# Kernel optimization log

Hardware: AMD Instinct MI355X
Metric: run time of the kernel (lower is better)

## Reference

```python
import jax, jax.numpy as jnp
import numpy as np

HIDDEN = 1024
NUM_HEADS = 16
GROUP_SIZE = 2
GROUP_NUM = NUM_HEADS // GROUP_SIZE
HEAD_DIM = HIDDEN // NUM_HEADS


def setup_inputs() -> dict:
    key = jax.random.key(0)
    ks = jax.random.split(key, 9)
    B, S = 1, 4096
    s = 0.02
    return {
        "hidden_state": jax.random.normal(ks[0], (B, S, HIDDEN), jnp.float32),
        "Wq": jax.random.normal(ks[1], (HIDDEN, HIDDEN), jnp.float32) * s,
        "bq": jnp.zeros((HIDDEN,), jnp.float32),
        "Wk": jax.random.normal(ks[2], (HIDDEN, GROUP_NUM * HEAD_DIM), jnp.float32) * s,
        "bk": jnp.zeros((GROUP_NUM * HEAD_DIM,), jnp.float32),
        "Wv": jax.random.normal(ks[3], (HIDDEN, GROUP_NUM * HEAD_DIM), jnp.float32) * s,
        "bv": jnp.zeros((GROUP_NUM * HEAD_DIM,), jnp.float32),
        "Wo": jax.random.normal(ks[4], (HIDDEN, HIDDEN), jnp.float32) * s,
        "bo": jnp.zeros((HIDDEN,), jnp.float32),
    }


def reference(hidden_state, Wq, bq, Wk, bk, Wv, bv, Wo, bo):
    B, S, _ = hidden_state.shape
    # projections
    q = hidden_state @ Wq + bq                      # [B,S,H*hd]
    k = hidden_state @ Wk + bk                      # [B,S,G*hd]
    v = hidden_state @ Wv + bv                      # [B,S,G*hd]
    q = q.reshape(B, S, NUM_HEADS, HEAD_DIM).transpose(0, 2, 1, 3)   # [B,H,S,hd]
    k = k.reshape(B, S, GROUP_NUM, HEAD_DIM).transpose(0, 2, 1, 3)   # [B,G,S,hd]
    v = v.reshape(B, S, GROUP_NUM, HEAD_DIM).transpose(0, 2, 1, 3)
    # expand KV heads: each kv head repeated group_size times consecutively
    k = jnp.repeat(k, GROUP_SIZE, axis=1)           # [B,H,S,hd]
    v = jnp.repeat(v, GROUP_SIZE, axis=1)
    scale = 1.0 / np.sqrt(HEAD_DIM).astype(np.float32)
    scores = jnp.einsum('bhqd,bhkd->bhqk', q, k) * scale   # [B,H,S,S]
    attn = jax.nn.softmax(scores, axis=-1)
    ctx = jnp.einsum('bhqk,bhkd->bhqd', attn, v)    # [B,H,S,hd]
    ctx = ctx.transpose(0, 2, 1, 3).reshape(B, S, HIDDEN)
    return ctx @ Wo + bo
```

## Files before the change

kernel.cpp:

```cpp
#include <hip/hip_runtime.h>
#include <hip/hip_bf16.h>
#include <cstdint>
#include <cstddef>

typedef __bf16 bf16x8 __attribute__((ext_vector_type(8)));
typedef float f32x4 __attribute__((ext_vector_type(4)));
typedef float f32x16 __attribute__((ext_vector_type(16)));
typedef uint32_t u32x4 __attribute__((ext_vector_type(4)));
typedef __hip_bfloat16 bf16h;

__device__ __forceinline__ unsigned short bf16bits(float f) {
  bf16h h = __float2bfloat16(f);
  return __builtin_bit_cast(unsigned short, h);
}

__global__ void cast_f32_bf16(const float* __restrict__ src, bf16h* __restrict__ dst, int n) {
  int i = (blockIdx.x * blockDim.x + threadIdx.x) * 4;
  if (i >= n) return;
  float4 v = *reinterpret_cast<const float4*>(src + i);
  ushort4 o;
  o.x = bf16bits(v.x); o.y = bf16bits(v.y); o.z = bf16bits(v.z); o.w = bf16bits(v.w);
  *reinterpret_cast<ushort4*>(dst + i) = o;
}

__global__ void transpose_cast_f32(const float* __restrict__ src, bf16h* __restrict__ dst,
                                   int R, int C, float scale) {
  __shared__ float tile[32][33];
  int c0 = blockIdx.x * 32, r0 = blockIdx.y * 32;
  int tx = threadIdx.x, ty = threadIdx.y;
  #pragma unroll
  for (int i = 0; i < 32; i += 8)
    tile[ty + i][tx] = src[(size_t)(r0 + ty + i) * C + c0 + tx];
  __syncthreads();
  #pragma unroll
  for (int i = 0; i < 32; i += 8)
    dst[(size_t)(c0 + ty + i) * R + r0 + tx] = __float2bfloat16(tile[tx][ty + i] * scale);
}

__global__ void transpose_bf16_tile(const bf16h* __restrict__ src, bf16h* __restrict__ dst,
                                    int R, int ldsrc, int col0) {
  __shared__ bf16h tile[32][33];
  int c0 = blockIdx.x * 32, r0 = blockIdx.y * 32;
  int tx = threadIdx.x, ty = threadIdx.y;
  #pragma unroll
  for (int i = 0; i < 32; i += 8)
    tile[ty + i][tx] = src[(size_t)(r0 + ty + i) * ldsrc + col0 + c0 + tx];
  __syncthreads();
  #pragma unroll
  for (int i = 0; i < 32; i += 8)
    dst[(size_t)(c0 + ty + i) * R + r0 + tx] = tile[tx][ty + i];
}

__global__ void concat_bias(const float* __restrict__ bq, const float* __restrict__ bk,
                            const float* __restrict__ bv, float* __restrict__ bcat, float qscale) {
  int i = blockIdx.x * blockDim.x + threadIdx.x;
  if (i >= 2048) return;
  bcat[i] = (i < 1024) ? bq[i] * qscale : (i < 1536 ? bk[i - 1024] : bv[i - 1536]);
}

__device__ __forceinline__ void store_out(float* p, float v) { *p = v; }
__device__ __forceinline__ void store_out(bf16h* p, float v) { *p = __float2bfloat16(v); }

template <typename OutT>
__global__ __launch_bounds__(256) void gemm_bt(const bf16h* __restrict__ A, const bf16h* __restrict__ BT,
                                               const float* __restrict__ bias, OutT* __restrict__ C,
                                               int M, int N, int K) {
  __shared__ __align__(16) bf16h As[128 * 64];
  __shared__ __align__(16) bf16h Bs[128 * 64];
  const int tid = threadIdx.x;
  const int lane = tid & 63;
  const int m0 = blockIdx.y * 128, n0 = blockIdx.x * 128;
  const int wid = tid >> 6, wr = wid >> 1, wc = wid & 1;
  const int cl = lane & 15, rg = lane >> 4;
  const int srow = tid >> 3, scol = (tid & 7) * 8;
  f32x4 acc[4][4] = {};

  for (int k0 = 0; k0 < K; k0 += 64) {
    __syncthreads();
    #pragma unroll
    for (int i = 0; i < 4; ++i) {
      int r = i * 32 + srow;
      __builtin_amdgcn_global_load_lds(
          (__attribute__((address_space(1))) void*)(A + (size_t)(m0 + r) * K + k0 + scol),
          (__attribute__((address_space(3))) void*)(As + i * 2048 + tid * 8), 16, 0, 0);
    }
    #pragma unroll
    for (int i = 0; i < 4; ++i) {
      int r = i * 32 + srow;
      __builtin_amdgcn_global_load_lds(
          (__attribute__((address_space(1))) void*)(BT + (size_t)(n0 + r) * K + k0 + scol),
          (__attribute__((address_space(3))) void*)(Bs + i * 2048 + tid * 8), 16, 0, 0);
    }
    __syncthreads();
    #pragma unroll
    for (int ks = 0; ks < 2; ++ks) {
      bf16x8 af[4], bfr[4];
      #pragma unroll
      for (int mi = 0; mi < 4; ++mi)
        af[mi] = *reinterpret_cast<const bf16x8*>(As + (wr * 64 + mi * 16 + cl) * 64 + ks * 32 + rg * 8);
      #pragma unroll
      for (int ni = 0; ni < 4; ++ni)
        bfr[ni] = *reinterpret_cast<const bf16x8*>(Bs + (wc * 64 + ni * 16 + cl) * 64 + ks * 32 + rg * 8);
      #pragma unroll
      for (int mi = 0; mi < 4; ++mi)
        #pragma unroll
        for (int ni = 0; ni < 4; ++ni)
          acc[mi][ni] = __builtin_amdgcn_mfma_f32_16x16x32_bf16(af[mi], bfr[ni], acc[mi][ni], 0, 0, 0);
    }
  }
  #pragma unroll
  for (int ni = 0; ni < 4; ++ni) {
    int col = n0 + wc * 64 + ni * 16 + cl;
    float bv = bias[col];
    #pragma unroll
    for (int mi = 0; mi < 4; ++mi) {
      #pragma unroll
      for (int j = 0; j < 4; ++j) {
        int row = m0 + wr * 64 + mi * 16 + rg * 4 + j;
        store_out(&C[(size_t)row * N + col], acc[mi][ni][j] + bv);
      }
    }
  }
}

__global__ __launch_bounds__(256, 2) void attn_fwd(const bf16h* __restrict__ qkv,
                                                   const bf16h* __restrict__ vt,
                                                   bf16h* __restrict__ ctx) {
  __shared__ __align__(16) char smem[32768];
  const int tid = threadIdx.x, lane = tid & 63, wid = tid >> 6;
  const int l31 = lane & 31, hi = lane >> 5;
  const int h = blockIdx.y, g = h >> 1;
  const int q0 = blockIdx.x * 128 + wid * 32;

  bf16x8 qf[4];
  {
    const bf16h* qrow = qkv + (size_t)(q0 + l31) * 2048 + h * 64 + hi * 8;
    #pragma unroll
    for (int ds = 0; ds < 4; ++ds)
      qf[ds] = *reinterpret_cast<const bf16x8*>(qrow + ds * 16);
  }

  u32x4 onesw; onesw[0] = 0x3F803F80u; onesw[1] = 0x3F803F80u; onesw[2] = 0x3F803F80u; onesw[3] = 0x3F803F80u;
  const bf16x8 onesf = __builtin_bit_cast(bf16x8, onesw);

  f32x16 oacc[2], lacc;
  #pragma unroll
  for (int i = 0; i < 16; ++i) { oacc[0][i] = 0.f; oacc[1][i] = 0.f; lacc[i] = 0.f; }

  auto stage = [&](int kk, int b) {
    char* kb = smem + b * 16384;
    char* vb = kb + 8192;
    #pragma unroll
    for (int i = 0; i < 2; ++i) {
      int slot = tid + i * 256;
      int r = slot >> 3, s = slot & 7, sx = s ^ (r & 7);
      __builtin_amdgcn_global_load_lds(
          (__attribute__((address_space(1))) void*)(qkv + (size_t)(kk + r) * 2048 + 1024 + g * 64 + sx * 8),
          (__attribute__((address_space(3))) void*)(kb + slot * 16), 16, 0, 0);
      __builtin_amdgcn_global_load_lds(
          (__attribute__((address_space(1))) void*)(vt + (size_t)(g * 64 + r) * 4096 + kk + sx * 8),
          (__attribute__((address_space(3))) void*)(vb + slot * 16), 16, 0, 0);
    }
  };

  stage(0, 0);
  __syncthreads();
  int cur = 0;

  auto pv_slice = [&](int ks, const f32x16& S, const char* vb) {
    const int u = ks & 1;
    uint32_t w0, w1, w2, w3;
    asm("v_cvt_pk_bf16_f32 %0, %1, %2" : "=v"(w0) : "v"(S[8 * u + 0]), "v"(S[8 * u + 1]));
    asm("v_cvt_pk_bf16_f32 %0, %1, %2" : "=v"(w1) : "v"(S[8 * u + 2]), "v"(S[8 * u + 3]));
    asm("v_cvt_pk_bf16_f32 %0, %1, %2" : "=v"(w2) : "v"(S[8 * u + 4]), "v"(S[8 * u + 5]));
    asm("v_cvt_pk_bf16_f32 %0, %1, %2" : "=v"(w3) : "v"(S[8 * u + 6]), "v"(S[8 * u + 7]));
    asm("v_permlane32_swap_b32 %0, %1" : "+v"(w0), "+v"(w2));
    asm("v_permlane32_swap_b32 %0, %1" : "+v"(w1), "+v"(w3));
    u32x4 pw; pw[0] = w0; pw[1] = w1; pw[2] = w2; pw[3] = w3;
    bf16x8 pa = __builtin_bit_cast(bf16x8, pw);
    int cb = 32 * ks + 16 * hi;
    #pragma unroll
    for (int dh = 0; dh < 2; ++dh) {
      int r = dh * 32 + l31;
      bf16x8 vf = *reinterpret_cast<const bf16x8*>(vb + ((r * 128 + cb) ^ ((r & 7) << 4)));
      oacc[dh] = __builtin_amdgcn_mfma_f32_32x32x16_bf16(vf, pa, oacc[dh], 0, 0, 0);
    }
    lacc = __builtin_amdgcn_mfma_f32_32x32x16_bf16(onesf, pa, lacc, 0, 0, 0);
  };

  for (int tt = 0; tt < 64; ++tt) {
    if (tt < 63) stage((tt + 1) * 64, cur ^ 1);
    const char* kb = smem + cur * 16384;
    const char* vb = kb + 8192;

    f32x16 s0, s1;
    #pragma unroll
    for (int i = 0; i < 16; ++i) { s0[i] = 0.f; s1[i] = 0.f; }
    __builtin_amdgcn_s_setprio(1);
    #pragma unroll
    for (int ds = 0; ds < 4; ++ds) {
      int cb = 32 * ds + 16 * hi;
      int r0 = l31, r1 = 32 + l31;
      bf16x8 k0 = *reinterpret_cast<const bf16x8*>(kb + ((r0 * 128 + cb) ^ ((r0 & 7) << 4)));
      bf16x8 k1 = *reinterpret_cast<const bf16x8*>(kb + ((r1 * 128 + cb) ^ ((r1 & 7) << 4)));
      s0 = __builtin_amdgcn_mfma_f32_32x32x16_bf16(k0, qf[ds], s0, 0, 0, 0);
      s1 = __builtin_amdgcn_mfma_f32_32x32x16_bf16(k1, qf[ds], s1, 0, 0, 0);
    }
    __builtin_amdgcn_s_setprio(0);

    #pragma unroll
    for (int r = 0; r < 16; ++r) {
      s0[r] = __builtin_amdgcn_exp2f(s0[r]);
      s1[r] = __builtin_amdgcn_exp2f(s1[r]);
    }

    __builtin_amdgcn_s_setprio(1);
    pv_slice(0, s0, vb);
    pv_slice(1, s0, vb);
    pv_slice(2, s1, vb);
    pv_slice(3, s1, vb);
    __builtin_amdgcn_s_setprio(0);

    __syncthreads();
    cur ^= 1;
  }

  float inv = 1.0f / lacc[0];
  #pragma unroll
  for (int dh = 0; dh < 2; ++dh)
    #pragma unroll
    for (int r = 0; r < 16; ++r) {
      int d = dh * 32 + (r & 3) + 8 * (r >> 2) + 4 * hi;
      ctx[(size_t)(q0 + l31) * 1024 + h * 64 + d] = __float2bfloat16(oacc[dh][r] * inv);
    }
}

extern "C" void kernel_launch(void* const* d_in, const int* in_sizes, int n_in,
                              void* d_out, int out_size, void* d_ws, size_t ws_size,
                              hipStream_t stream) {
  const float* hs = (const float*)d_in[0];
  const float* Wq = (const float*)d_in[1];
  const float* bq = (const float*)d_in[2];
  const float* Wk = (const float*)d_in[3];
  const float* bk = (const float*)d_in[4];
  const float* Wv = (const float*)d_in[5];
  const float* bv = (const float*)d_in[6];
  const float* Wo = (const float*)d_in[7];
  const float* bo = (const float*)d_in[8];
  float* out = (float*)d_out;

  const float QSCALE = 0.125f * 1.44269504088896f;

  char* ws = (char*)d_ws;
  bf16h* hb   = (bf16h*)(ws);
  bf16h* WcT  = (bf16h*)(ws + (8u  << 20));
  bf16h* WoT  = (bf16h*)(ws + (12u << 20));
  bf16h* qkv  = (bf16h*)(ws + (14u << 20));
  bf16h* vtg  = (bf16h*)(ws + (30u << 20));
  bf16h* ctx  = (bf16h*)(ws + (34u << 20));
  float* bcat = (float*)(ws + (42u << 20));

  cast_f32_bf16<<<dim3(4096), dim3(256), 0, stream>>>(hs, hb, 4096 * 1024);
  transpose_cast_f32<<<dim3(32, 32), dim3(32, 8), 0, stream>>>(Wq, WcT, 1024, 1024, QSCALE);
  transpose_cast_f32<<<dim3(16, 32), dim3(32, 8), 0, stream>>>(Wk, WcT + 1024 * 1024, 1024, 512, 1.0f);
  transpose_cast_f32<<<dim3(16, 32), dim3(32, 8), 0, stream>>>(Wv, WcT + 1536 * 1024, 1024, 512, 1.0f);
  transpose_cast_f32<<<dim3(32, 32), dim3(32, 8), 0, stream>>>(Wo, WoT, 1024, 1024, 1.0f);
  concat_bias<<<dim3(8), dim3(256), 0, stream>>>(bq, bk, bv, bcat, QSCALE);
  gemm_bt<bf16h><<<dim3(16, 32), dim3(256), 0, stream>>>(hb, WcT, bcat, qkv, 4096, 2048, 1024);
  transpose_bf16_tile<<<dim3(16, 128), dim3(32, 8), 0, stream>>>(qkv, vtg, 4096, 2048, 1536);
  attn_fwd<<<dim3(32, 16), dim3(256), 0, stream>>>(qkv, vtg, ctx);
  gemm_bt<float><<<dim3(8, 32), dim3(256), 0, stream>>>(ctx, WoT, bo, out, 4096, 1024, 1024);
}
```

Before: 157.1 us.

## Fuse V transpose into QKV GEMM epilogue and split attention keys across two chunks

Result: no change. 158.5 us (+0.9%).

```diff
diff --git a/kernel.cpp b/kernel.cpp
--- a/kernel.cpp
+++ b/kernel.cpp
@@ -12,6 +12,9 @@
 __device__ __forceinline__ unsigned short bf16bits(float f) {
   bf16h h = __float2bfloat16(f);
   return __builtin_bit_cast(unsigned short, h);
+}
+__device__ __forceinline__ float bf16tof(unsigned short u) {
+  union { uint32_t i; float f; } v; v.i = (uint32_t)u << 16; return v.f;
 }
 
 __global__ void cast_f32_bf16(const float* __restrict__ src, bf16h* __restrict__ dst, int n) {
@@ -37,20 +40,6 @@
     dst[(size_t)(c0 + ty + i) * R + r0 + tx] = __float2bfloat16(tile[tx][ty + i] * scale);
 }
 
-__global__ void transpose_bf16_tile(const bf16h* __restrict__ src, bf16h* __restrict__ dst,
-                                    int R, int ldsrc, int col0) {
-  __shared__ bf16h tile[32][33];
-  int c0 = blockIdx.x * 32, r0 = blockIdx.y * 32;
-  int tx = threadIdx.x, ty = threadIdx.y;
-  #pragma unroll
-  for (int i = 0; i < 32; i += 8)
-    tile[ty + i][tx] = src[(size_t)(r0 + ty + i) * ldsrc + col0 + c0 + tx];
-  __syncthreads();
-  #pragma unroll
-  for (int i = 0; i < 32; i += 8)
-    dst[(size_t)(c0 + ty + i) * R + r0 + tx] = tile[tx][ty + i];
-}
-
 __global__ void concat_bias(const float* __restrict__ bq, const float* __restrict__ bk,
                             const float* __restrict__ bv, float* __restrict__ bcat, float qscale) {
   int i = blockIdx.x * blockDim.x + threadIdx.x;
@@ -64,6 +53,7 @@
 template <typename OutT>
 __global__ __launch_bounds__(256) void gemm_bt(const bf16h* __restrict__ A, const bf16h* __restrict__ BT,
                                                const float* __restrict__ bias, OutT* __restrict__ C,
+                                               int ldc, bf16h* __restrict__ vtg, int vcol0,
                                                int M, int N, int K) {
   __shared__ __align__(16) bf16h As[128 * 64];
   __shared__ __align__(16) bf16h Bs[128 * 64];
@@ -108,44 +98,65 @@
           acc[mi][ni] = __builtin_amdgcn_mfma_f32_16x16x32_bf16(af[mi], bfr[ni], acc[mi][ni], 0, 0, 0);
     }
   }
-  #pragma unroll
-  for (int ni = 0; ni < 4; ++ni) {
-    int col = n0 + wc * 64 + ni * 16 + cl;
-    float bv = bias[col];
-    #pragma unroll
-    for (int mi = 0; mi < 4; ++mi) {
-      #pragma unroll
-      for (int j = 0; j < 4; ++j) {
-        int row = m0 + wr * 64 + mi * 16 + rg * 4 + j;
-        store_out(&C[(size_t)row * N + col], acc[mi][ni][j] + bv);
+  if (n0 >= vcol0) {
+    #pragma unroll
+    for (int ni = 0; ni < 4; ++ni) {
+      int col = n0 + wc * 64 + ni * 16 + cl;
+      float bv = bias[col];
+      #pragma unroll
+      for (int mi = 0; mi < 4; ++mi) {
+        int row0 = m0 + wr * 64 + mi * 16 + rg * 4;
+        ushort4 o;
+        o.x = bf16bits(acc[mi][ni][0] + bv);
+        o.y = bf16bits(acc[mi][ni][1] + bv);
+        o.z = bf16bits(acc[mi][ni][2] + bv);
+        o.w = bf16bits(acc[mi][ni][3] + bv);
+        *reinterpret_cast<ushort4*>(vtg + (size_t)(col - vcol0) * 4096 + row0) = o;
       }
     }
-  }
-}
-
-__global__ __launch_bounds__(256, 2) void attn_fwd(const bf16h* __restrict__ qkv,
+  } else {
+    #pragma unroll
+    for (int ni = 0; ni < 4; ++ni) {
+      int col = n0 + wc * 64 + ni * 16 + cl;
+      float bv = bias[col];
+      #pragma unroll
+      for (int mi = 0; mi < 4; ++mi) {
+        #pragma unroll
+        for (int j = 0; j < 4; ++j) {
+          int row = m0 + wr * 64 + mi * 16 + rg * 4 + j;
+          store_out(&C[(size_t)row * ldc + col], acc[mi][ni][j] + bv);
+        }
+      }
+    }
+  }
+}
+
+__global__ __launch_bounds__(256, 2) void attn_fwd(const bf16h* __restrict__ qk,
                                                    const bf16h* __restrict__ vt,
-                                                   bf16h* __restrict__ ctx) {
+                                                   bf16h* __restrict__ part,
+                                                   float* __restrict__ lpart) {
   __shared__ __align__(16) char smem[32768];
   const int tid = threadIdx.x, lane = tid & 63, wid = tid >> 6;
   const int l31 = lane & 31, hi = lane >> 5;
-  const int h = blockIdx.y, g = h >> 1;
-  const int q0 = blockIdx.x * 128 + wid * 32;
-
-  bf16x8 qf[4];
+  const int h = blockIdx.y, g = h >> 1, c = blockIdx.z;
+  const int q0 = blockIdx.x * 256 + wid * 64;
+  const int kbase = c * 2048;
+
+  bf16x8 qfA[4], qfB[4];
   {
-    const bf16h* qrow = qkv + (size_t)(q0 + l31) * 2048 + h * 64 + hi * 8;
-    #pragma unroll
-    for (int ds = 0; ds < 4; ++ds)
-      qf[ds] = *reinterpret_cast<const bf16x8*>(qrow + ds * 16);
-  }
-
-  u32x4 onesw; onesw[0] = 0x3F803F80u; onesw[1] = 0x3F803F80u; onesw[2] = 0x3F803F80u; onesw[3] = 0x3F803F80u;
-  const bf16x8 onesf = __builtin_bit_cast(bf16x8, onesw);
-
-  f32x16 oacc[2], lacc;
+    const bf16h* qrowA = qk + (size_t)(q0 + l31) * 1536 + h * 64 + hi * 8;
+    const bf16h* qrowB = qrowA + (size_t)32 * 1536;
+    #pragma unroll
+    for (int ds = 0; ds < 4; ++ds) {
+      qfA[ds] = *reinterpret_cast<const bf16x8*>(qrowA + ds * 16);
+      qfB[ds] = *reinterpret_cast<const bf16x8*>(qrowB + ds * 16);
+    }
+  }
+
+  f32x16 oA0, oA1, oB0, oB1;
   #pragma unroll
-  for (int i = 0; i < 16; ++i) { oacc[0][i] = 0.f; oacc[1][i] = 0.f; lacc[i] = 0.f; }
+  for (int i = 0; i < 16; ++i) { oA0[i] = 0.f; oA1[i] = 0.f; oB0[i] = 0.f; oB1[i] = 0.f; }
+  float lsumA = 0.f, lsumB = 0.f;
 
   auto stage = [&](int kk, int b) {
     char* kb = smem + b * 16384;
@@ -155,7 +166,7 @@
       int slot = tid + i * 256;
       int r = slot >> 3, s = slot & 7, sx = s ^ (r & 7);
       __builtin_amdgcn_global_load_lds(
-          (__attribute__((address_space(1))) void*)(qkv + (size_t)(kk + r) * 2048 + 1024 + g * 64 + sx * 8),
+          (__attribute__((address_space(1))) void*)(qk + (size_t)(kk + r) * 1536 + 1024 + g * 64 + sx * 8),
           (__attribute__((address_space(3))) void*)(kb + slot * 16), 16, 0, 0);
       __builtin_amdgcn_global_load_lds(
           (__attribute__((address_space(1))) void*)(vt + (size_t)(g * 64 + r) * 4096 + kk + sx * 8),
@@ -163,12 +174,11 @@
     }
   };
 
-  stage(0, 0);
+  stage(kbase, 0);
   __syncthreads();
   int cur = 0;
 
-  auto pv_slice = [&](int ks, const f32x16& S, const char* vb) {
-    const int u = ks & 1;
+  auto build_pa = [&](const f32x16& S, int u) -> bf16x8 {
     uint32_t w0, w1, w2, w3;
     asm("v_cvt_pk_bf16_f32 %0, %1, %2" : "=v"(w0) : "v"(S[8 * u + 0]), "v"(S[8 * u + 1]));
     asm("v_cvt_pk_bf16_f32 %0, %1, %2" : "=v"(w1) : "v"(S[8 * u + 2]), "v"(S[8 * u + 3]));
@@ -177,25 +187,17 @@
     asm("v_permlane32_swap_b32 %0, %1" : "+v"(w0), "+v"(w2));
     asm("v_permlane32_swap_b32 %0, %1" : "+v"(w1), "+v"(w3));
     u32x4 pw; pw[0] = w0; pw[1] = w1; pw[2] = w2; pw[3] = w3;
-    bf16x8 pa = __builtin_bit_cast(bf16x8, pw);
-    int cb = 32 * ks + 16 * hi;
-    #pragma unroll
-    for (int dh = 0; dh < 2; ++dh) {
-      int r = dh * 32 + l31;
-      bf16x8 vf = *reinterpret_cast<const bf16x8*>(vb + ((r * 128 + cb) ^ ((r & 7) << 4)));
-      oacc[dh] = __builtin_amdgcn_mfma_f32_32x32x16_bf16(vf, pa, oacc[dh], 0, 0, 0);
-    }
-    lacc = __builtin_amdgcn_mfma_f32_32x32x16_bf16(onesf, pa, lacc, 0, 0, 0);
+    return __builtin_bit_cast(bf16x8, pw);
   };
 
-  for (int tt = 0; tt < 64; ++tt) {
-    if (tt < 63) stage((tt + 1) * 64, cur ^ 1);
+  for (int tt = 0; tt < 32; ++tt) {
+    if (tt < 31) stage(kbase + (tt + 1) * 64, cur ^ 1);
     const char* kb = smem + cur * 16384;
     const char* vb = kb + 8192;
 
-    f32x16 s0, s1;
-    #pragma unroll
-    for (int i = 0; i < 16; ++i) { s0[i] = 0.f; s1[i] = 0.f; }
+    f32x16 sA0, sA1, sB0, sB1;
+    #pragma unroll
+    for (int i = 0; i < 16; ++i) { sA0[i] = 0.f; sA1[i] = 0.f; sB0[i] = 0.f; sB1[i] = 0.f; }
     __builtin_amdgcn_s_setprio(1);
     #pragma unroll
     for (int ds = 0; ds < 4; ++ds) {
@@ -203,36 +205,99 @@
       int r0 = l31, r1 = 32 + l31;
       bf16x8 k0 = *reinterpret_cast<const bf16x8*>(kb + ((r0 * 128 + cb) ^ ((r0 & 7) << 4)));
       bf16x8 k1 = *reinterpret_cast<const bf16x8*>(kb + ((r1 * 128 + cb) ^ ((r1 & 7) << 4)));
-      s0 = __builtin_amdgcn_mfma_f32_32x32x16_bf16(k0, qf[ds], s0, 0, 0, 0);
-      s1 = __builtin_amdgcn_mfma_f32_32x32x16_bf16(k1, qf[ds], s1, 0, 0, 0);
+      sA0 = __builtin_amdgcn_mfma_f32_32x32x16_bf16(k0, qfA[ds], sA0, 0, 0, 0);
+      sA1 = __builtin_amdgcn_mfma_f32_32x32x16_bf16(k1, qfA[ds], sA1, 0, 0, 0);
+      sB0 = __builtin_amdgcn_mfma_f32_32x32x16_bf16(k0, qfB[ds], sB0, 0, 0, 0);
+      sB1 = __builtin_amdgcn_mfma_f32_32x32x16_bf16(k1, qfB[ds], sB1, 0, 0, 0);
     }
     __builtin_amdgcn_s_setprio(0);
 
+    float rsA = 0.f, rsB = 0.f;
     #pragma unroll
     for (int r = 0; r < 16; ++r) {
-      s0[r] = __builtin_amdgcn_exp2f(s0[r]);
-      s1[r] = __builtin_amdgcn_exp2f(s1[r]);
-    }
+      sA0[r] = __builtin_amdgcn_exp2f(sA0[r]); rsA += sA0[r];
+      sA1[r] = __builtin_amdgcn_exp2f(sA1[r]); rsA += sA1[r];
+      sB0[r] = __builtin_amdgcn_exp2f(sB0[r]); rsB += sB0[r];
+      sB1[r] = __builtin_amdgcn_exp2f(sB1[r]); rsB += sB1[r];
+    }
+    lsumA += rsA + __shfl_xor(rsA, 32);
+    lsumB += rsB + __shfl_xor(rsB, 32);
 
     __builtin_amdgcn_s_setprio(1);
-    pv_slice(0, s0, vb);
-    pv_slice(1, s0, vb);
-    pv_slice(2, s1, vb);
-    pv_slice(3, s1, vb);
+    #pragma unroll
+    for (int ks = 0; ks < 4; ++ks) {
+      const int u = ks & 1;
+      bf16x8 paA = build_pa(ks < 2 ? sA0 : sA1, u);
+      bf16x8 paB = build_pa(ks < 2 ? sB0 : sB1, u);
+      int cb = 32 * ks + 16 * hi;
+      int r0 = l31, r1 = 32 + l31;
+      bf16x8 vf0 = *reinterpret_cast<const bf16x8*>(vb + ((r0 * 128 + cb) ^ ((r0 & 7) << 4)));
+      bf16x8 vf1 = *reinterpret_cast<const bf16x8*>(vb + ((r1 * 128 + cb) ^ ((r1 & 7) << 4)));
+      oA0 = __builtin_amdgcn_mfma_f32_32x32x16_bf16(vf0, paA, oA0, 0, 0, 0);
+      oA1 = __builtin_amdgcn_mfma_f32_32x32x16_bf16(vf1, paA, oA1, 0, 0, 0);
+      oB0 = __builtin_amdgcn_mfma_f32_32x32x16_bf16(vf0, paB, oB0, 0, 0, 0);
+      oB1 = __builtin_amdgcn_mfma_f32_32x32x16_bf16(vf1, paB, oB1, 0, 0, 0);
+    }
     __builtin_amdgcn_s_setprio(0);
 
     __syncthreads();
     cur ^= 1;
   }
 
-  float inv = 1.0f / lacc[0];
+  {
+    int qA = q0 + l31, qB = qA + 32;
+    bf16h* pA = part + ((size_t)(c * 4096 + qA) * 16 + h) * 64;
+    bf16h* pB = part + ((size_t)(c * 4096 + qB) * 16 + h) * 64;
+    #pragma unroll
+    for (int dh = 0; dh < 2; ++dh) {
+      const f32x16& aA = dh ? oA1 : oA0;
+      const f32x16& aB = dh ? oB1 : oB0;
+      #pragma unroll
+      for (int t = 0; t < 4; ++t) {
+        int d0 = dh * 32 + 8 * t + 4 * hi;
+        ushort4 sa, sb;
+        sa.x = bf16bits(aA[4 * t + 0]); sa.y = bf16bits(aA[4 * t + 1]);
+        sa.z = bf16bits(aA[4 * t + 2]); sa.w = bf16bits(aA[4 * t + 3]);
+        sb.x = bf16bits(aB[4 * t + 0]); sb.y = bf16bits(aB[4 * t + 1]);
+        sb.z = bf16bits(aB[4 * t + 2]); sb.w = bf16bits(aB[4 * t + 3]);
+        *reinterpret_cast<ushort4*>(pA + d0) = sa;
+        *reinterpret_cast<ushort4*>(pB + d0) = sb;
+      }
+    }
+    if (hi == 0) {
+      lpart[(size_t)(c * 4096 + qA) * 16 + h] = lsumA;
+      lpart[(size_t)(c * 4096 + qB) * 16 + h] = lsumB;
+    }
+  }
+}
+
+__global__ __launch_bounds__(256) void combine_part(const bf16h* __restrict__ part,
+                                                    const float* __restrict__ lpart,
+                                                    bf16h* __restrict__ ctx) {
+  int idx = blockIdx.x * 256 + threadIdx.x;
+  int q = idx >> 4, h = idx & 15;
+  const bf16h* p0 = part + ((size_t)q * 16 + h) * 64;
+  const bf16h* p1 = p0 + (size_t)4096 * 1024;
+  float inv = 1.0f / (lpart[(size_t)q * 16 + h] + lpart[(size_t)4096 * 16 + q * 16 + h]);
+  bf16h* o = ctx + (size_t)q * 1024 + h * 64;
   #pragma unroll
-  for (int dh = 0; dh < 2; ++dh)
-    #pragma unroll
-    for (int r = 0; r < 16; ++r) {
-      int d = dh * 32 + (r & 3) + 8 * (r >> 2) + 4 * hi;
-      ctx[(size_t)(q0 + l31) * 1024 + h * 64 + d] = __float2bfloat16(oacc[dh][r] * inv);
-    }
+  for (int w = 0; w < 8; ++w) {
+    ushort4 a = *reinterpret_cast<const ushort4*>(p0 + w * 8);
+    ushort4 b = *reinterpret_cast<const ushort4*>(p1 + w * 8);
+    ushort4 c2 = *reinterpret_cast<const ushort4*>(p0 + w * 8 + 4);
+    ushort4 d2 = *reinterpret_cast<const ushort4*>(p1 + w * 8 + 4);
+    ushort4 r0, r1;
+    r0.x = bf16bits((bf16tof(a.x) + bf16tof(b.x)) * inv);
+    r0.y = bf16bits((bf16tof(a.y) + bf16tof(b.y)) * inv);
+    r0.z = bf16bits((bf16tof(a.z) + bf16tof(b.z)) * inv);
+    r0.w = bf16bits((bf16tof(a.w) + bf16tof(b.w)) * inv);
+    r1.x = bf16bits((bf16tof(c2.x) + bf16tof(d2.x)) * inv);
+    r1.y = bf16bits((bf16tof(c2.y) + bf16tof(d2.y)) * inv);
+    r1.z = bf16bits((bf16tof(c2.z) + bf16tof(d2.z)) * inv);
+    r1.w = bf16bits((bf16tof(c2.w) + bf16tof(d2.w)) * inv);
+    *reinterpret_cast<ushort4*>(o + w * 8) = r0;
+    *reinterpret_cast<ushort4*>(o + w * 8 + 4) = r1;
+  }
 }
 
 extern "C" void kernel_launch(void* const* d_in, const int* in_sizes, int n_in,
@@ -252,13 +317,16 @@
   const float QSCALE = 0.125f * 1.44269504088896f;
 
   char* ws = (char*)d_ws;
-  bf16h* hb   = (bf16h*)(ws);
-  bf16h* WcT  = (bf16h*)(ws + (8u  << 20));
-  bf16h* WoT  = (bf16h*)(ws + (12u << 20));
-  bf16h* qkv  = (bf16h*)(ws + (14u << 20));
-  bf16h* vtg  = (bf16h*)(ws + (30u << 20));
-  bf16h* ctx  = (bf16h*)(ws + (34u << 20));
-  float* bcat = (float*)(ws + (42u << 20));
+  const size_t MB = 1u << 20;
+  bf16h* hb    = (bf16h*)(ws);
+  bf16h* WcT   = (bf16h*)(ws + 8 * MB);
+  bf16h* part  = (bf16h*)(ws);
+  float* lpart = (float*)(ws + 16 * MB);
+  bf16h* qk    = (bf16h*)(ws + 17 * MB);
+  bf16h* ctx   = (bf16h*)(ws + 17 * MB);
+  bf16h* vtg   = (bf16h*)(ws + 29 * MB);
+  bf16h* WoT   = (bf16h*)(ws + 33 * MB);
+  float* bcat  = (float*)(ws + 35 * MB);
 
   cast_f32_bf16<<<dim3(4096), dim3(256), 0, stream>>>(hs, hb, 4096 * 1024);
   transpose_cast_f32<<<dim3(32, 32), dim3(32, 8), 0, stream>>>(Wq, WcT, 1024, 1024, QSCALE);
@@ -266,8 +334,10 @@
   transpose_cast_f32<<<dim3(16, 32), dim3(32, 8), 0, stream>>>(Wv, WcT + 1536 * 1024, 1024, 512, 1.0f);
   transpose_cast_f32<<<dim3(32, 32), dim3(32, 8), 0, stream>>>(Wo, WoT, 1024, 1024, 1.0f);
   concat_bias<<<dim3(8), dim3(256), 0, stream>>>(bq, bk, bv, bcat, QSCALE);
-  gemm_bt<bf16h><<<dim3(16, 32), dim3(256), 0, stream>>>(hb, WcT, bcat, qkv, 4096, 2048, 1024);
-  transpose_bf16_tile<<<dim3(16, 128), dim3(32, 8), 0, stream>>>(qkv, vtg, 4096, 2048, 1536);
-  attn_fwd<<<dim3(32, 16), dim3(256), 0, stream>>>(qkv, vtg, ctx);
-  gemm_bt<float><<<dim3(8, 32), dim3(256), 0, stream>>>(ctx, WoT, bo, out, 4096, 1024, 1024);
-}
+  gemm_bt<bf16h><<<dim3(16, 32), dim3(256), 0, stream>>>(hb, WcT, bcat, qk, 1536, vtg, 1536,
+                                                         4096, 2048, 1024);
+  attn_fwd<<<dim3(16, 16, 2), dim3(256), 0, stream>>>(qk, vtg, part, lpart);
+  combine_part<<<dim3(256), dim3(256), 0, stream>>>(part, lpart, ctx);
+  gemm_bt<float><<<dim3(8, 32), dim3(256), 0, stream>>>(ctx, WoT, bo, out, 1024, (bf16h*)nullptr,
+                                                        0x40000000, 4096, 1024, 1024);
+}
```
